# Performance work log

Measured on AMD Instinct MI355X. Metric: run time of the kernel, lower is better.

The kernel has to match this reference:

```python
import jax, jax.numpy as jnp
import numpy as np

NUM_HEADS = 16
HEIGHT = 32
WIDTH = 32
FEATURES_DIM = HEIGHT * WIDTH  # 1024
EMBED_DIM = 1024


def setup_inputs() -> dict:
    key = jax.random.key(0)
    ks = jax.random.split(key, 9)
    s_in = 1.0 / np.sqrt(FEATURES_DIM)
    s_e = 1.0 / np.sqrt(EMBED_DIM)
    return {
        "x": jax.random.normal(ks[0], (16, 512, HEIGHT, WIDTH), dtype=jnp.float32),
        "Wq": jax.random.uniform(ks[1], (EMBED_DIM, FEATURES_DIM), jnp.float32, -s_in, s_in),
        "bq": jax.random.uniform(ks[2], (EMBED_DIM,), jnp.float32, -s_in, s_in),
        "Wk": jax.random.uniform(ks[3], (EMBED_DIM, FEATURES_DIM), jnp.float32, -s_in, s_in),
        "bk": jax.random.uniform(ks[4], (EMBED_DIM,), jnp.float32, -s_in, s_in),
        "Wv": jax.random.uniform(ks[5], (EMBED_DIM, FEATURES_DIM), jnp.float32, -s_in, s_in),
        "bv": jax.random.uniform(ks[6], (EMBED_DIM,), jnp.float32, -s_in, s_in),
        "Wo": jax.random.uniform(ks[7], (FEATURES_DIM, EMBED_DIM), jnp.float32, -s_e, s_e),
        "bo": jax.random.uniform(ks[8], (FEATURES_DIM,), jnp.float32, -s_e, s_e),
    }


def reference(x, Wq, bq, Wk, bk, Wv, bv, Wo, bo):
    B, C, H, W = x.shape
    nh = NUM_HEADS
    hd = EMBED_DIM // nh
    xf = x.reshape(B, C, H * W)  # [B, C, F] - channel tokens
    q = xf @ Wq.T + bq  # [B, C, E]
    k = xf @ Wk.T + bk
    v = xf @ Wv.T + bv
    q = q.reshape(B, C, nh, hd).transpose(0, 2, 1, 3)  # [B, nh, C, hd]
    k = k.reshape(B, C, nh, hd).transpose(0, 2, 1, 3)
    v = v.reshape(B, C, nh, hd).transpose(0, 2, 1, 3)
    scores = jnp.einsum("bhcd,bhkd->bhck", q, k) / jnp.sqrt(jnp.float32(hd))
    attn = jax.nn.softmax(scores, axis=-1)
    out = jnp.einsum("bhck,bhkd->bhcd", attn, v)  # [B, nh, C, hd]
    out = out.transpose(0, 2, 1, 3).reshape(B, C, EMBED_DIM)
    out = out @ Wo.T + bo  # [B, C, F]
    return out.reshape(B, C, H, W)
```

## Files before the change

kernel.cpp:

```cpp
#include <hip/hip_runtime.h>


typedef unsigned short u16;
typedef __attribute__((ext_vector_type(8))) short short8;
typedef __attribute__((ext_vector_type(4))) float f32x4;
typedef __attribute__((ext_vector_type(4))) unsigned short u16x4;

__device__ __forceinline__ u16 f2bf(float x) {
  unsigned u = __float_as_uint(x);
  u += 0x7FFFu + ((u >> 16) & 1u);
  return (u16)(u >> 16);
}

__device__ __forceinline__ void async16(const void* g, void* l) {
  __builtin_amdgcn_global_load_lds(
      (__attribute__((address_space(1))) unsigned int*)(g),
      (__attribute__((address_space(3))) unsigned int*)(l), 16, 0, 0);
}

__global__ __launch_bounds__(256) void cvt_bf16(const float* __restrict__ s,
                                                u16* __restrict__ d, int n4) {
  int i = blockIdx.x * 256 + threadIdx.x;
  if (i >= n4) return;
  f32x4 v = ((const f32x4*)s)[i];
  u16x4 o;
#pragma unroll
  for (int j = 0; j < 4; ++j) o[j] = f2bf(v[j]);
  ((u16x4*)d)[i] = o;
}

__device__ __forceinline__ void gemm_tile(const u16* __restrict__ A,
                                          const u16* __restrict__ W,
                                          u16* lA, u16* lB,
                                          int m0, int n0, f32x4 acc[4][4]) {
  const int t = threadIdx.x;
  const int wave = t >> 6, lane = t & 63, lr = lane & 15, lg = lane >> 4;
  const int wr = wave >> 1, wc = wave & 1;
  const u16* ga = A + (m0 + (t >> 2)) * 1024 + (t & 3) * 8;
  const u16* gb = W + (n0 + (t >> 2)) * 1024 + (t & 3) * 8;
  u16* la0 = lA + wave * 512;
  u16* la1 = lA + 2048 + wave * 512;
  u16* lb0 = lB + wave * 512;
  u16* lb1 = lB + 2048 + wave * 512;
  const u16* pa = lA + (wr * 64 + lr) * 32 + lg * 8;
  const u16* pb = lB + (wc * 64 + lr) * 32 + lg * 8;

  for (int k0 = 0; k0 < 1024; k0 += 32) {
    __syncthreads();
    async16(ga + k0, la0);
    async16(ga + 65536 + k0, la1);
    async16(gb + k0, lb0);
    async16(gb + 65536 + k0, lb1);
    __syncthreads();
    short8 av[4], bv[4];
#pragma unroll
    for (int i = 0; i < 4; ++i) av[i] = *(const short8*)(pa + i * 512);
#pragma unroll
    for (int i = 0; i < 4; ++i) bv[i] = *(const short8*)(pb + i * 512);
#pragma unroll
    for (int i = 0; i < 4; ++i)
#pragma unroll
      for (int j = 0; j < 4; ++j)
        acc[i][j] = __builtin_amdgcn_mfma_f32_16x16x32_bf16(av[i], bv[j],
                                                            acc[i][j], 0, 0, 0);
  }
}

__global__ __launch_bounds__(256) void gemm_qkv(
    const u16* __restrict__ xb, const u16* __restrict__ wq,
    const u16* __restrict__ wk, const u16* __restrict__ wv,
    const float* __restrict__ bq, const float* __restrict__ bk,
    const float* __restrict__ bv, u16* __restrict__ qo, u16* __restrict__ ko,
    u16* __restrict__ vo) {
  __shared__ u16 lA[4096], lB[4096];
  const int z = blockIdx.z;
  const u16* W = (z == 0) ? wq : (z == 1) ? wk : wv;
  const float* bias = (z == 0) ? bq : (z == 1) ? bk : bv;
  u16* outp = (z == 0) ? qo : (z == 1) ? ko : vo;
  const int m0 = blockIdx.y * 128, n0 = blockIdx.x * 128;
  f32x4 acc[4][4];
#pragma unroll
  for (int i = 0; i < 4; ++i)
#pragma unroll
    for (int j = 0; j < 4; ++j) acc[i][j] = (f32x4){0.f, 0.f, 0.f, 0.f};
  gemm_tile(xb, W, lA, lB, m0, n0, acc);

  const int t = threadIdx.x;
  const int wave = t >> 6, lane = t & 63, lr = lane & 15, lg = lane >> 4;
  const int wr = wave >> 1, wc = wave & 1;
  float bb[4];
#pragma unroll
  for (int cb = 0; cb < 4; ++cb) bb[cb] = bias[n0 + wc * 64 + cb * 16 + lr];
#pragma unroll
  for (int rb = 0; rb < 4; ++rb)
#pragma unroll
    for (int cb = 0; cb < 4; ++cb)
#pragma unroll
      for (int r = 0; r < 4; ++r) {
        int m = m0 + wr * 64 + rb * 16 + lg * 4 + r;
        int n = n0 + wc * 64 + cb * 16 + lr;
        float val = acc[rb][cb][r] + bb[cb];
        int b_ = m >> 9, c = m & 511, h = n >> 6, dd = n & 63;
        int idx = (z == 2) ? ((((b_ << 4) + h) << 15) + (dd << 9) + c)
                           : ((((b_ << 4) + h) << 15) + (c << 6) + dd);
        outp[idx] = f2bf(val);
      }
}

__global__ __launch_bounds__(256) void gemm_oproj(const u16* __restrict__ ab,
                                                  const u16* __restrict__ wo,
                                                  const float* __restrict__ bo,
                                                  float* __restrict__ out) {
  __shared__ u16 lA[4096], lB[4096];
  const int m0 = blockIdx.y * 128, n0 = blockIdx.x * 128;
  f32x4 acc[4][4];
#pragma unroll
  for (int i = 0; i < 4; ++i)
#pragma unroll
    for (int j = 0; j < 4; ++j) acc[i][j] = (f32x4){0.f, 0.f, 0.f, 0.f};
  gemm_tile(ab, wo, lA, lB, m0, n0, acc);

  const int t = threadIdx.x;
  const int wave = t >> 6, lane = t & 63, lr = lane & 15, lg = lane >> 4;
  const int wr = wave >> 1, wc = wave & 1;
  float bb[4];
#pragma unroll
  for (int cb = 0; cb < 4; ++cb) bb[cb] = bo[n0 + wc * 64 + cb * 16 + lr];
#pragma unroll
  for (int rb = 0; rb < 4; ++rb)
#pragma unroll
    for (int cb = 0; cb < 4; ++cb)
#pragma unroll
      for (int r = 0; r < 4; ++r) {
        int m = m0 + wr * 64 + rb * 16 + lg * 4 + r;
        int n = n0 + wc * 64 + cb * 16 + lr;
        out[m * 1024 + n] = acc[rb][cb][r] + bb[cb];
      }
}

__global__ __launch_bounds__(512, 2) void attn_kernel(
    const u16* __restrict__ qb, const u16* __restrict__ kb,
    const u16* __restrict__ vb, u16* __restrict__ ab) {
  __shared__ u16 lK[32768];
  __shared__ u16 lV[32768];
  __shared__ u16 lP[8192];
  const int t = threadIdx.x;
  const int bh = blockIdx.x;
  const int b_ = bh >> 4, h_ = bh & 15;
  const u16* kg = kb + bh * 32768;
  const u16* vg = vb + bh * 32768;
#pragma unroll
  for (int i = 0; i < 8; ++i) {
    int row = i * 64 + (t >> 3), slot = t & 7;
    short8 kv = *(const short8*)(kg + row * 64 + slot * 8);
    *(short8*)(lK + row * 64 + ((slot ^ (row & 7)) << 3)) = kv;
    int vrow = i * 8 + (t >> 6), vslot = t & 63;
    short8 vv = *(const short8*)(vg + vrow * 512 + vslot * 8);
    *(short8*)(lV + vrow * 512 + ((vslot ^ (vrow & 7)) << 3)) = vv;
  }
  __syncthreads();

  const int wv_ = t >> 6, lane = t & 63, lr = lane & 15, lg = lane >> 4;
  u16* lPw = lP + wv_ * 1024;
  const u16* qg = qb + bh * 32768;
  const float sc = 0.125f * 1.44269504088896f;

#pragma unroll 1
  for (int qi = 0; qi < 4; ++qi) {
    const int qrow = (wv_ * 4 + qi) * 16;
    short8 a0 = *(const short8*)(qg + (qrow + lr) * 64 + lg * 8);
    short8 a1 = *(const short8*)(qg + (qrow + lr) * 64 + 32 + lg * 8);
    f32x4 s[32];
#pragma unroll
    for (int f = 0; f < 32; ++f) {
      const u16* kr = lK + (f * 16 + lr) * 64;
      short8 k0 = *(const short8*)(kr + ((lg ^ (lr & 7)) << 3));
      short8 k1 = *(const short8*)(kr + (((4 + lg) ^ (lr & 7)) << 3));
      f32x4 z4 = (f32x4){0.f, 0.f, 0.f, 0.f};
      z4 = __builtin_amdgcn_mfma_f32_16x16x32_bf16(a0, k0, z4, 0, 0, 0);
      z4 = __builtin_amdgcn_mfma_f32_16x16x32_bf16(a1, k1, z4, 0, 0, 0);
      s[f] = z4;
    }
    float inv[4];
#pragma unroll
    for (int r = 0; r < 4; ++r) {
      float m_ = s[0][r];
#pragma unroll
      for (int f = 1; f < 32; ++f) m_ = fmaxf(m_, s[f][r]);
      m_ = fmaxf(m_, __shfl_xor(m_, 1));
      m_ = fmaxf(m_, __shfl_xor(m_, 2));
      m_ = fmaxf(m_, __shfl_xor(m_, 4));
      m_ = fmaxf(m_, __shfl_xor(m_, 8));
      float sm = 0.f;
#pragma unroll
      for (int f = 0; f < 32; ++f) {
        float e = exp2f((s[f][r] - m_) * sc);
        s[f][r] = e;
        sm += e;
      }
      sm += __shfl_xor(sm, 1);
      sm += __shfl_xor(sm, 2);
      sm += __shfl_xor(sm, 4);
      sm += __shfl_xor(sm, 8);
      inv[r] = 1.f / sm;
    }
    f32x4 o[4];
#pragma unroll
    for (int i = 0; i < 4; ++i) o[i] = (f32x4){0.f, 0.f, 0.f, 0.f};
#pragma unroll
    for (int ch = 0; ch < 8; ++ch) {
#pragma unroll
      for (int cf = 0; cf < 4; ++cf)
#pragma unroll
        for (int r = 0; r < 4; ++r) {
          int q = lg * 4 + r, kc = cf * 16 + lr;
          lPw[q * 64 + (((kc >> 3) ^ (q & 7)) << 3) + (kc & 7)] =
              f2bf(s[ch * 4 + cf][r]);
        }
      asm volatile("s_waitcnt lgkmcnt(0)" ::: "memory");
      const u16* pr = lPw + lr * 64;
      short8 pa0 = *(const short8*)(pr + ((lg ^ (lr & 7)) << 3));
      short8 pa1 = *(const short8*)(pr + (((4 + lg) ^ (lr & 7)) << 3));
#pragma unroll
      for (int df = 0; df < 4; ++df) {
        const u16* vr = lV + (df * 16 + lr) * 512;
        short8 v0 = *(const short8*)(vr + (((ch * 8 + lg) ^ (lr & 7)) << 3));
        short8 v1 =
            *(const short8*)(vr + (((ch * 8 + 4 + lg) ^ (lr & 7)) << 3));
        o[df] = __builtin_amdgcn_mfma_f32_16x16x32_bf16(pa0, v0, o[df], 0, 0, 0);
        o[df] = __builtin_amdgcn_mfma_f32_16x16x32_bf16(pa1, v1, o[df], 0, 0, 0);
      }
    }
#pragma unroll
    for (int df = 0; df < 4; ++df)
#pragma unroll
      for (int r = 0; r < 4; ++r) {
        int q = qrow + lg * 4 + r, dd = df * 16 + lr;
        ab[(b_ * 512 + q) * 1024 + h_ * 64 + dd] = f2bf(o[df][r] * inv[r]);
      }
  }
}

extern "C" void kernel_launch(void* const* d_in, const int* in_sizes, int n_in,
                              void* d_out, int out_size, void* d_ws,
                              size_t ws_size, hipStream_t stream) {
  (void)in_sizes; (void)n_in; (void)out_size;
  const float* x  = (const float*)d_in[0];
  const float* Wq = (const float*)d_in[1];
  const float* bq = (const float*)d_in[2];
  const float* Wk = (const float*)d_in[3];
  const float* bk = (const float*)d_in[4];
  const float* Wv = (const float*)d_in[5];
  const float* bv = (const float*)d_in[6];
  const float* Wo = (const float*)d_in[7];
  const float* bo = (const float*)d_in[8];
  float* out = (float*)d_out;

  if (ws_size < 75497472u) return;
  u16* xb  = (u16*)d_ws;
  u16* wqb = xb + 8388608;
  u16* wkb = wqb + 1048576;
  u16* wvb = wkb + 1048576;
  u16* wob = wvb + 1048576;
  u16* qbuf = wob + 1048576;
  u16* kbuf = qbuf + 8388608;
  u16* vbuf = kbuf + 8388608;
  u16* abuf = xb;

  cvt_bf16<<<8192, 256, 0, stream>>>(x, xb, 2097152);
  cvt_bf16<<<1024, 256, 0, stream>>>(Wq, wqb, 262144);
  cvt_bf16<<<1024, 256, 0, stream>>>(Wk, wkb, 262144);
  cvt_bf16<<<1024, 256, 0, stream>>>(Wv, wvb, 262144);
  cvt_bf16<<<1024, 256, 0, stream>>>(Wo, wob, 262144);

  gemm_qkv<<<dim3(8, 64, 3), 256, 0, stream>>>(xb, wqb, wkb, wvb, bq, bk, bv,
                                               qbuf, kbuf, vbuf);
  attn_kernel<<<256, 512, 0, stream>>>(qbuf, kbuf, vbuf, abuf);
  gemm_oproj<<<dim3(8, 64, 1), 256, 0, stream>>>(abuf, wob, bo, out);
}
```

Measured before the change: 182.2 us.

## Rewrite GEMMs as 8-wave 128x256 tiles with triple-buffered async LDS pipeline

Replaces the simple double-sync GEMM loop with an 8-wave, 128x256 output tile per block. It uses a triple-buffered LDS pipeline with K=64 stages issued via global_load_lds, interleaved with MFMA phases. It also adds an XOR swizzle on LDS to avoid bank conflicts, s_setprio around MFMA bursts, and an XCD-aware block remapping across the 8 dies. The aim is to hide global-load latency and cut the barrier overhead per MFMA. In exchange it uses much more LDS per block (one block per CU) and adds many barriers.

```diff
diff --git a/kernel.cpp b/kernel.cpp
--- a/kernel.cpp
+++ b/kernel.cpp
@@ -5,6 +5,8 @@
 typedef __attribute__((ext_vector_type(8))) short short8;
 typedef __attribute__((ext_vector_type(4))) float f32x4;
 typedef __attribute__((ext_vector_type(4))) unsigned short u16x4;
+
+#define MFMA16(a, b, c) __builtin_amdgcn_mfma_f32_16x16x32_bf16(a, b, c, 0, 0, 0)
 
 __device__ __forceinline__ u16 f2bf(float x) {
   unsigned u = __float_as_uint(x);
@@ -29,77 +31,147 @@
   ((u16x4*)d)[i] = o;
 }
 
-__device__ __forceinline__ void gemm_tile(const u16* __restrict__ A,
-                                          const u16* __restrict__ W,
-                                          u16* lA, u16* lB,
-                                          int m0, int n0, f32x4 acc[4][4]) {
+__device__ __forceinline__ void gemm8(const u16* __restrict__ A,
+                                      const u16* __restrict__ W,
+                                      int m0, int n0, u16* lds,
+                                      f32x4 acc[4][4]) {
   const int t = threadIdx.x;
   const int wave = t >> 6, lane = t & 63, lr = lane & 15, lg = lane >> 4;
-  const int wr = wave >> 1, wc = wave & 1;
-  const u16* ga = A + (m0 + (t >> 2)) * 1024 + (t & 3) * 8;
-  const u16* gb = W + (n0 + (t >> 2)) * 1024 + (t & 3) * 8;
-  u16* la0 = lA + wave * 512;
-  u16* la1 = lA + 2048 + wave * 512;
-  u16* lb0 = lB + wave * 512;
-  u16* lb1 = lB + 2048 + wave * 512;
-  const u16* pa = lA + (wr * 64 + lr) * 32 + lg * 8;
-  const u16* pb = lB + (wc * 64 + lr) * 32 + lg * 8;
-
-  for (int k0 = 0; k0 < 1024; k0 += 32) {
-    __syncthreads();
-    async16(ga + k0, la0);
-    async16(ga + 65536 + k0, la1);
-    async16(gb + k0, lb0);
-    async16(gb + 65536 + k0, lb1);
-    __syncthreads();
-    short8 av[4], bv[4];
-#pragma unroll
-    for (int i = 0; i < 4; ++i) av[i] = *(const short8*)(pa + i * 512);
-#pragma unroll
-    for (int i = 0; i < 4; ++i) bv[i] = *(const short8*)(pb + i * 512);
-#pragma unroll
-    for (int i = 0; i < 4; ++i)
-#pragma unroll
-      for (int j = 0; j < 4; ++j)
-        acc[i][j] = __builtin_amdgcn_mfma_f32_16x16x32_bf16(av[i], bv[j],
-                                                            acc[i][j], 0, 0, 0);
-  }
-}
-
-__global__ __launch_bounds__(256) void gemm_qkv(
+  const int wr = wave >> 2, wn = wave & 3;
+  const int srow = t >> 3;
+  const int scol = ((t & 7) ^ ((t >> 3) & 7)) << 3;
+  const u16* gA = A + (size_t)(m0 + srow) * 1024 + scol;
+  const u16* gB = W + (size_t)(n0 + srow) * 1024 + scol;
+  u16* stA = lds + wave * 512;
+  u16* stB = lds + 8192 + wave * 512;
+  const int aoff = (wr * 64 + lr) * 64;
+  const int boff = (wn * 64 + lr) * 64;
+  const int sw0 = (lg ^ (lr & 7)) << 3;
+  const int sw1 = ((4 ^ lg) ^ (lr & 7)) << 3;
+
+#define STAGEA(buf, k0)                                   \
+  {                                                       \
+    async16(gA + (k0), stA + (buf) * 24576);              \
+    async16(gA + 65536 + (k0), stA + (buf) * 24576 + 4096); \
+  }
+#define STAGEB2(buf, k0, j)                                             \
+  {                                                                     \
+    async16(gB + (j) * 65536 + (k0), stB + (buf) * 24576 + (j) * 4096); \
+    async16(gB + ((j) + 1) * 65536 + (k0),                              \
+            stB + (buf) * 24576 + ((j) + 1) * 4096);                    \
+  }
+
+  STAGEA(0, 0); STAGEB2(0, 0, 0); STAGEB2(0, 0, 2);
+  STAGEA(1, 64); STAGEB2(1, 64, 0); STAGEB2(1, 64, 2);
+  asm volatile("s_waitcnt vmcnt(6)" ::: "memory");
+  __builtin_amdgcn_s_barrier();
+
+#pragma unroll
+  for (int tt = 0; tt < 16; ++tt) {
+    const int cb = tt % 3, nb = (tt + 2) % 3;
+    const bool st = (tt < 14);
+    const int kn = (tt + 2) * 64;
+    const u16* la = lds + cb * 24576 + aoff;
+    const u16* lb = lds + cb * 24576 + 8192 + boff;
+    short8 av[4], b0, b1;
+#pragma unroll
+    for (int m = 0; m < 4; ++m) av[m] = *(const short8*)(la + m * 1024 + sw0);
+    b0 = *(const short8*)(lb + 0 * 1024 + sw0);
+    b1 = *(const short8*)(lb + 1 * 1024 + sw0);
+    if (st) STAGEA(nb, kn);
+    __builtin_amdgcn_s_barrier();
+    __builtin_amdgcn_s_setprio(1);
+#pragma unroll
+    for (int m = 0; m < 4; ++m) {
+      acc[m][0] = MFMA16(av[m], b0, acc[m][0]);
+      acc[m][1] = MFMA16(av[m], b1, acc[m][1]);
+    }
+    __builtin_amdgcn_s_setprio(0);
+    __builtin_amdgcn_s_barrier();
+    b0 = *(const short8*)(lb + 2 * 1024 + sw0);
+    b1 = *(const short8*)(lb + 3 * 1024 + sw0);
+    if (st) STAGEB2(nb, kn, 0);
+    __builtin_amdgcn_s_barrier();
+    __builtin_amdgcn_s_setprio(1);
+#pragma unroll
+    for (int m = 0; m < 4; ++m) {
+      acc[m][2] = MFMA16(av[m], b0, acc[m][2]);
+      acc[m][3] = MFMA16(av[m], b1, acc[m][3]);
+    }
+    __builtin_amdgcn_s_setprio(0);
+    __builtin_amdgcn_s_barrier();
+#pragma unroll
+    for (int m = 0; m < 4; ++m) av[m] = *(const short8*)(la + m * 1024 + sw1);
+    b0 = *(const short8*)(lb + 0 * 1024 + sw1);
+    b1 = *(const short8*)(lb + 1 * 1024 + sw1);
+    if (st) STAGEB2(nb, kn, 2);
+    __builtin_amdgcn_s_barrier();
+    __builtin_amdgcn_s_setprio(1);
+#pragma unroll
+    for (int m = 0; m < 4; ++m) {
+      acc[m][0] = MFMA16(av[m], b0, acc[m][0]);
+      acc[m][1] = MFMA16(av[m], b1, acc[m][1]);
+    }
+    __builtin_amdgcn_s_setprio(0);
+    __builtin_amdgcn_s_barrier();
+    b0 = *(const short8*)(lb + 2 * 1024 + sw1);
+    b1 = *(const short8*)(lb + 3 * 1024 + sw1);
+    __builtin_amdgcn_s_barrier();
+    __builtin_amdgcn_s_setprio(1);
+#pragma unroll
+    for (int m = 0; m < 4; ++m) {
+      acc[m][2] = MFMA16(av[m], b0, acc[m][2]);
+      acc[m][3] = MFMA16(av[m], b1, acc[m][3]);
+    }
+    __builtin_amdgcn_s_setprio(0);
+    if (tt < 14) {
+      asm volatile("s_waitcnt vmcnt(6)" ::: "memory");
+    } else {
+      asm volatile("s_waitcnt vmcnt(0)" ::: "memory");
+    }
+    __builtin_amdgcn_s_barrier();
+  }
+#undef STAGEA
+#undef STAGEB2
+}
+
+__global__ __launch_bounds__(512, 1) void gemm_qkv(
     const u16* __restrict__ xb, const u16* __restrict__ wq,
     const u16* __restrict__ wk, const u16* __restrict__ wv,
     const float* __restrict__ bq, const float* __restrict__ bk,
     const float* __restrict__ bv, u16* __restrict__ qo, u16* __restrict__ ko,
     u16* __restrict__ vo) {
-  __shared__ u16 lA[4096], lB[4096];
-  const int z = blockIdx.z;
+  __shared__ u16 lds[73728];
+  const int id = blockIdx.x;
+  const int lid = (id & 7) * 96 + (id >> 3);
+  const int z = lid >> 8;
+  const int rem = lid & 255;
+  const int m0 = (rem >> 2) * 128, n0 = (rem & 3) * 256;
   const u16* W = (z == 0) ? wq : (z == 1) ? wk : wv;
   const float* bias = (z == 0) ? bq : (z == 1) ? bk : bv;
   u16* outp = (z == 0) ? qo : (z == 1) ? ko : vo;
-  const int m0 = blockIdx.y * 128, n0 = blockIdx.x * 128;
   f32x4 acc[4][4];
 #pragma unroll
   for (int i = 0; i < 4; ++i)
 #pragma unroll
     for (int j = 0; j < 4; ++j) acc[i][j] = (f32x4){0.f, 0.f, 0.f, 0.f};
-  gemm_tile(xb, W, lA, lB, m0, n0, acc);
+  gemm8(xb, W, m0, n0, lds, acc);
 
   const int t = threadIdx.x;
   const int wave = t >> 6, lane = t & 63, lr = lane & 15, lg = lane >> 4;
-  const int wr = wave >> 1, wc = wave & 1;
+  const int wr = wave >> 2, wn = wave & 3;
   float bb[4];
 #pragma unroll
-  for (int cb = 0; cb < 4; ++cb) bb[cb] = bias[n0 + wc * 64 + cb * 16 + lr];
-#pragma unroll
-  for (int rb = 0; rb < 4; ++rb)
-#pragma unroll
-    for (int cb = 0; cb < 4; ++cb)
+  for (int nf = 0; nf < 4; ++nf) bb[nf] = bias[n0 + wn * 64 + nf * 16 + lr];
+#pragma unroll
+  for (int mf = 0; mf < 4; ++mf)
+#pragma unroll
+    for (int nf = 0; nf < 4; ++nf)
 #pragma unroll
       for (int r = 0; r < 4; ++r) {
-        int m = m0 + wr * 64 + rb * 16 + lg * 4 + r;
-        int n = n0 + wc * 64 + cb * 16 + lr;
-        float val = acc[rb][cb][r] + bb[cb];
+        int m = m0 + wr * 64 + mf * 16 + lg * 4 + r;
+        int n = n0 + wn * 64 + nf * 16 + lr;
+        float val = acc[mf][nf][r] + bb[nf];
         int b_ = m >> 9, c = m & 511, h = n >> 6, dd = n & 63;
         int idx = (z == 2) ? ((((b_ << 4) + h) << 15) + (dd << 9) + c)
                            : ((((b_ << 4) + h) << 15) + (c << 6) + dd);
@@ -107,34 +179,36 @@
       }
 }
 
-__global__ __launch_bounds__(256) void gemm_oproj(const u16* __restrict__ ab,
-                                                  const u16* __restrict__ wo,
-                                                  const float* __restrict__ bo,
-                                                  float* __restrict__ out) {
-  __shared__ u16 lA[4096], lB[4096];
-  const int m0 = blockIdx.y * 128, n0 = blockIdx.x * 128;
+__global__ __launch_bounds__(512, 1) void gemm_oproj(const u16* __restrict__ ab,
+                                                     const u16* __restrict__ wo,
+                                                     const float* __restrict__ bo,
+                                                     float* __restrict__ out) {
+  __shared__ u16 lds[73728];
+  const int id = blockIdx.x;
+  const int lid = (id & 7) * 32 + (id >> 3);
+  const int m0 = (lid >> 2) * 128, n0 = (lid & 3) * 256;
   f32x4 acc[4][4];
 #pragma unroll
   for (int i = 0; i < 4; ++i)
 #pragma unroll
     for (int j = 0; j < 4; ++j) acc[i][j] = (f32x4){0.f, 0.f, 0.f, 0.f};
-  gemm_tile(ab, wo, lA, lB, m0, n0, acc);
+  gemm8(ab, wo, m0, n0, lds, acc);
 
   const int t = threadIdx.x;
   const int wave = t >> 6, lane = t & 63, lr = lane & 15, lg = lane >> 4;
-  const int wr = wave >> 1, wc = wave & 1;
+  const int wr = wave >> 2, wn = wave & 3;
   float bb[4];
 #pragma unroll
-  for (int cb = 0; cb < 4; ++cb) bb[cb] = bo[n0 + wc * 64 + cb * 16 + lr];
-#pragma unroll
-  for (int rb = 0; rb < 4; ++rb)
-#pragma unroll
-    for (int cb = 0; cb < 4; ++cb)
+  for (int nf = 0; nf < 4; ++nf) bb[nf] = bo[n0 + wn * 64 + nf * 16 + lr];
+#pragma unroll
+  for (int mf = 0; mf < 4; ++mf)
+#pragma unroll
+    for (int nf = 0; nf < 4; ++nf)
 #pragma unroll
       for (int r = 0; r < 4; ++r) {
-        int m = m0 + wr * 64 + rb * 16 + lg * 4 + r;
-        int n = n0 + wc * 64 + cb * 16 + lr;
-        out[m * 1024 + n] = acc[rb][cb][r] + bb[cb];
+        int m = m0 + wr * 64 + mf * 16 + lg * 4 + r;
+        int n = n0 + wn * 64 + nf * 16 + lr;
+        out[m * 1024 + n] = acc[mf][nf][r] + bb[nf];
       }
 }
 
@@ -177,8 +251,8 @@
       short8 k0 = *(const short8*)(kr + ((lg ^ (lr & 7)) << 3));
       short8 k1 = *(const short8*)(kr + (((4 + lg) ^ (lr & 7)) << 3));
       f32x4 z4 = (f32x4){0.f, 0.f, 0.f, 0.f};
-      z4 = __builtin_amdgcn_mfma_f32_16x16x32_bf16(a0, k0, z4, 0, 0, 0);
-      z4 = __builtin_amdgcn_mfma_f32_16x16x32_bf16(a1, k1, z4, 0, 0, 0);
+      z4 = MFMA16(a0, k0, z4);
+      z4 = MFMA16(a1, k1, z4);
       s[f] = z4;
     }
     float inv[4];
@@ -227,8 +301,8 @@
         short8 v0 = *(const short8*)(vr + (((ch * 8 + lg) ^ (lr & 7)) << 3));
         short8 v1 =
             *(const short8*)(vr + (((ch * 8 + 4 + lg) ^ (lr & 7)) << 3));
-        o[df] = __builtin_amdgcn_mfma_f32_16x16x32_bf16(pa0, v0, o[df], 0, 0, 0);
-        o[df] = __builtin_amdgcn_mfma_f32_16x16x32_bf16(pa1, v1, o[df], 0, 0, 0);
+        o[df] = MFMA16(pa0, v0, o[df]);
+        o[df] = MFMA16(pa1, v1, o[df]);
       }
     }
 #pragma unroll
@@ -273,8 +347,8 @@
   cvt_bf16<<<1024, 256, 0, stream>>>(Wv, wvb, 262144);
   cvt_bf16<<<1024, 256, 0, stream>>>(Wo, wob, 262144);
 
-  gemm_qkv<<<dim3(8, 64, 3), 256, 0, stream>>>(xb, wqb, wkb, wvb, bq, bk, bv,
-                                               qbuf, kbuf, vbuf);
+  gemm_qkv<<<768, 512, 0, stream>>>(xb, wqb, wkb, wvb, bq, bk, bv,
+                                    qbuf, kbuf, vbuf);
   attn_kernel<<<256, 512, 0, stream>>>(qbuf, kbuf, vbuf, abuf);
-  gemm_oproj<<<dim3(8, 64, 1), 256, 0, stream>>>(abuf, wob, bo, out);
-}
+  gemm_oproj<<<256, 512, 0, stream>>>(abuf, wob, bo, out);
+}
```

After: 174.3 us. 4.3% less time.
